# Performance work log

Measured on AMD Instinct MI355X. Metric: run time of the kernel, lower is better.

## Reference

```python
import jax, jax.numpy as jnp
import numpy as np

B, T, C, H, NUM_EDGE_TYPES = 2, 512, 256, 8, 16


def setup_inputs() -> dict:
    key = jax.random.key(0)
    ks = jax.random.split(key, 8)
    init = 0.02
    x = jax.random.normal(ks[0], (B, T, C), dtype=jnp.float32)
    bias_matrix = jax.random.randint(ks[1], (B, T, T), 0, NUM_EDGE_TYPES)
    w_attn = jax.random.normal(ks[2], (C, 3 * C), dtype=jnp.float32) * init
    w_proj = jax.random.normal(ks[3], (C, C), dtype=jnp.float32) * init
    w_edge_k = jax.random.normal(ks[4], (C, C), dtype=jnp.float32) * init
    w_edge_v = jax.random.normal(ks[5], (C, C), dtype=jnp.float32) * init
    edge_emb_table = jax.random.normal(ks[6], (NUM_EDGE_TYPES, C), dtype=jnp.float32)
    attn_bias_table = jax.random.normal(ks[7], (NUM_EDGE_TYPES, H), dtype=jnp.float32)
    return {
        "x": x,
        "bias_matrix": bias_matrix,
        "w_attn": w_attn,
        "w_proj": w_proj,
        "w_edge_k": w_edge_k,
        "w_edge_v": w_edge_v,
        "edge_emb_table": edge_emb_table,
        "attn_bias_table": attn_bias_table,
    }


def reference(x, bias_matrix, w_attn, w_proj, w_edge_k, w_edge_v,
              edge_emb_table, attn_bias_table):
    b, t, c = x.shape
    h = attn_bias_table.shape[1]
    e = c // h
    scale = jnp.sqrt(jnp.asarray(e, x.dtype))

    qkv = x @ w_attn                              # (B,T,3C)
    q, k, v = jnp.split(qkv, 3, axis=-1)
    # (B,H,T,E)
    q = q.reshape(b, t, h, e).transpose(0, 2, 1, 3)
    k = k.reshape(b, t, h, e).transpose(0, 2, 1, 3)
    v = v.reshape(b, t, h, e).transpose(0, 2, 1, 3)

    # edge-type embeddings and per-pair k/v modulation, (B,T,T,H,E)
    ee = edge_emb_table[bias_matrix]              # (B,T,T,C)
    e_k = (ee @ w_edge_k).reshape(b, t, t, h, e)
    e_v = (ee @ w_edge_v).reshape(b, t, t, h, e)

    # scores[b,h,i,j] = sum_e q[b,h,i,e] * k[b,h,j,e] * e_k[b, j, i, h, e]
    # (torch: e_k permuted to (B,H,j,i,E), broadcast-multiplied by k then
    #  contracted with q via 'bhie,bhjie->bhij')
    scores = jnp.einsum('bhie,bhje,bjihe->bhij', q, k, e_k) / scale

    causal = jnp.tril(jnp.ones((t, t), dtype=bool))  # (T,T)
    scores = jnp.where(causal, scores, -jnp.inf)

    # edge-type attention bias: (B,T,T,H) -> (B,H,T,T), zeroed above diagonal
    bias = attn_bias_table[bias_matrix].transpose(0, 3, 1, 2)
    bias = jnp.where(causal, bias, jnp.zeros((), bias.dtype))

    attn = jax.nn.softmax(scores + bias, axis=-1)  # (B,H,T,T)

    # y[b,h,i,e] = sum_j attn[b,h,i,j] * v[b,h,j,e] * e_v[b, j, i, h, e]
    y = jnp.einsum('bhij,bhje,bjihe->bhie', attn, v, e_v)
    y = y.transpose(0, 2, 1, 3).reshape(b, t, c)
    return y @ w_proj
```

## Files before the change

kernel.cpp:

```cpp
#include <hip/hip_runtime.h>
#include <hip/hip_bf16.h>
#include <math.h>

#define Bdim 2
#define Tdim 512
#define Cdim 256
#define Hdim 8
#define Edim 32
#define NTYPES 16
#define TI 8
#define JT 128

__global__ __launch_bounds__(256) void pre_kernel(
    const float* __restrict__ A, const float* __restrict__ Bw,
    const float* __restrict__ emb, const float* __restrict__ wk,
    const float* __restrict__ wv,
    float* __restrict__ qT, float* __restrict__ kT, float* __restrict__ vT,
    float* __restrict__ ekt, float* __restrict__ evt)
{
    __shared__ float smem[16 * 68 + 16 * 64];
    int tid = threadIdx.x;

    if (blockIdx.x >= 192) {
        int t = blockIdx.x - 192;
        float* se = smem;
        se[tid] = emb[t * Cdim + tid];
        __syncthreads();
        float a = 0.f, b = 0.f;
        for (int k = 0; k < Cdim; ++k) {
            float ev = se[k];
            a = fmaf(ev, wk[k * Cdim + tid], a);
            b = fmaf(ev, wv[k * Cdim + tid], b);
        }
        ekt[t * Cdim + tid] = a;
        evt[t * Cdim + tid] = b;
        return;
    }

    const int N = 3 * Cdim;
    const int K = Cdim;
    float (*As)[68] = (float(*)[68])smem;
    float (*Bs)[64] = (float(*)[64])(smem + 16 * 68);
    int m0 = (blockIdx.x / 12) * 64;
    int n0 = (blockIdx.x % 12) * 64;
    int tr = tid >> 4, tc = tid & 15;
    float acc[4][4] = {};
    int ar = tid >> 2, akq = (tid & 3) * 4;
    int bkr = tid >> 4, bcq = (tid & 15) * 4;

    for (int k0 = 0; k0 < K; k0 += 16) {
        float4 av = *(const float4*)(A + (size_t)(m0 + ar) * K + k0 + akq);
        float4 bv = *(const float4*)(Bw + (size_t)(k0 + bkr) * N + n0 + bcq);
        As[akq + 0][ar] = av.x;
        As[akq + 1][ar] = av.y;
        As[akq + 2][ar] = av.z;
        As[akq + 3][ar] = av.w;
        *(float4*)&Bs[bkr][bcq] = bv;
        __syncthreads();
#pragma unroll
        for (int kk = 0; kk < 16; ++kk) {
            float a0 = As[kk][tr * 4 + 0];
            float a1 = As[kk][tr * 4 + 1];
            float a2 = As[kk][tr * 4 + 2];
            float a3 = As[kk][tr * 4 + 3];
            float b0 = Bs[kk][tc * 4 + 0];
            float b1 = Bs[kk][tc * 4 + 1];
            float b2 = Bs[kk][tc * 4 + 2];
            float b3 = Bs[kk][tc * 4 + 3];
            acc[0][0] = fmaf(a0, b0, acc[0][0]);
            acc[0][1] = fmaf(a0, b1, acc[0][1]);
            acc[0][2] = fmaf(a0, b2, acc[0][2]);
            acc[0][3] = fmaf(a0, b3, acc[0][3]);
            acc[1][0] = fmaf(a1, b0, acc[1][0]);
            acc[1][1] = fmaf(a1, b1, acc[1][1]);
            acc[1][2] = fmaf(a1, b2, acc[1][2]);
            acc[1][3] = fmaf(a1, b3, acc[1][3]);
            acc[2][0] = fmaf(a2, b0, acc[2][0]);
            acc[2][1] = fmaf(a2, b1, acc[2][1]);
            acc[2][2] = fmaf(a2, b2, acc[2][2]);
            acc[2][3] = fmaf(a2, b3, acc[2][3]);
            acc[3][0] = fmaf(a3, b0, acc[3][0]);
            acc[3][1] = fmaf(a3, b1, acc[3][1]);
            acc[3][2] = fmaf(a3, b2, acc[3][2]);
            acc[3][3] = fmaf(a3, b3, acc[3][3]);
        }
        __syncthreads();
    }
#pragma unroll
    for (int i = 0; i < 4; ++i) {
#pragma unroll
        for (int j = 0; j < 4; ++j) {
            int m = m0 + tr * 4 + i;
            int n = n0 + tc * 4 + j;
            int b = m >> 9;
            int t = m & (Tdim - 1);
            int sec = n >> 8;
            int cc = n & (Cdim - 1);
            int h = cc >> 5;
            int e = cc & (Edim - 1);
            float* dst = (sec == 0) ? qT : (sec == 1) ? kT : vT;
            dst[(((size_t)b * Hdim + h) * Tdim + t) * Edim + e] = acc[i][j];
        }
    }
}

__global__ __launch_bounds__(512, 4) void attn_kernel(
    const float* __restrict__ qT, const float* __restrict__ kT,
    const float* __restrict__ vT, const int* __restrict__ bm,
    const float* __restrict__ ekt, const float* __restrict__ evt,
    const float* __restrict__ abt, float* __restrict__ y)
{
    __shared__ float kv[JT][36];
    __shared__ float qm[TI][NTYPES][36];
    __shared__ float ss[TI][516];
    __shared__ int   st1i[JT][17];
    __shared__ float sekt[NTYPES][36];
    __shared__ float sevt[NTYPES][36];
    __shared__ float sq[TI][36];
    __shared__ float sabt[NTYPES];
    __shared__ float sinv[TI];
    __shared__ float spartW[8][TI][Edim];

    const int pairIdx = blockIdx.x;
    const int bh = blockIdx.y;
    const int h = bh & (Hdim - 1);
    const int b = bh >> 3;
    const int tid = threadIdx.x;
    const int wave = tid >> 6;
    const int lane = tid & 63;
    const float inv_scale = 0.17677669529663687f;

    const float* qbase = qT + (size_t)bh * Tdim * Edim;
    const float* kbase = kT + (size_t)bh * Tdim * Edim;
    const float* vbase = vT + (size_t)bh * Tdim * Edim;
    const int* bmb = bm + (size_t)b * Tdim * Tdim;

    if (tid < 128) {
        int t = tid >> 3, eq = tid & 7;
        *(float4*)&sekt[t][eq * 4] = *(const float4*)&ekt[t * Cdim + h * Edim + eq * 4];
        *(float4*)&sevt[t][eq * 4] = *(const float4*)&evt[t * Cdim + h * Edim + eq * 4];
    }
    if (tid < NTYPES) sabt[tid] = abt[tid * Hdim + h];

    for (int rep = 0; rep < 2; ++rep) {
        int tau = rep ? (63 - pairIdx) : pairIdx;
        int i0 = tau * TI;
        int imax = i0 + TI - 1;
        int njt = (imax >> 7) + 1;

        __syncthreads();

        if (tid < TI * 8) {
            int r = tid >> 3, eq = tid & 7;
            *(float4*)&sq[r][eq * 4] =
                *(const float4*)&qbase[(size_t)(i0 + r) * Edim + eq * 4];
        }
        __syncthreads();
        for (int idx = tid; idx < TI * NTYPES * 8; idx += 512) {
            int eq = idx & 7;
            int t = (idx >> 3) & (NTYPES - 1);
            int r = idx >> 7;
            float4 qv = *(float4*)&sq[r][eq * 4];
            float4 ev = *(float4*)&sekt[t][eq * 4];
            float4 o;
            o.x = qv.x * ev.x; o.y = qv.y * ev.y;
            o.z = qv.z * ev.z; o.w = qv.w * ev.w;
            *(float4*)&qm[r][t][eq * 4] = o;
        }

        for (int jt = 0; jt < njt; ++jt) {
            int j0 = jt << 7;
            __syncthreads();
            for (int idx = tid; idx < JT * 8; idx += 512) {
                int r = idx >> 3, eq = idx & 7;
                *(float4*)&kv[r][eq * 4] =
                    *(const float4*)&kbase[(size_t)(j0 + r) * Edim + eq * 4];
            }
            if (tid < 256) {
                int r = tid >> 1, iq = (tid & 1) * 4;
                int4 bmv = *(const int4*)&bmb[(size_t)(j0 + r) * Tdim + i0 + iq];
                st1i[r][iq + 0] = bmv.x;
                st1i[r][iq + 1] = bmv.y;
                st1i[r][iq + 2] = bmv.z;
                st1i[r][iq + 3] = bmv.w;
            }
            __syncthreads();

            int jsub = wave & 1;
            int jl = (jsub << 6) + lane;
            int j = j0 + jl;
            float4 k4[8];
#pragma unroll
            for (int eq = 0; eq < 8; ++eq) k4[eq] = *(float4*)&kv[jl][eq * 4];

#pragma unroll
            for (int u = 0; u < 2; ++u) {
                int ii = (wave >> 1) + u * 4;
                int i = i0 + ii;
                if (j0 + (jsub << 6) > i) continue;
                int t1 = st1i[jl][ii];
                int t2 = bmb[(size_t)i * Tdim + j];
                float s = 0.f;
#pragma unroll
                for (int eq = 0; eq < 8; ++eq) {
                    float4 qv = *(float4*)&qm[ii][t1][eq * 4];
                    s = fmaf(qv.x, k4[eq].x, s);
                    s = fmaf(qv.y, k4[eq].y, s);
                    s = fmaf(qv.z, k4[eq].z, s);
                    s = fmaf(qv.w, k4[eq].w, s);
                }
                if (j <= i) ss[ii][j] = s * inv_scale + sabt[t2];
            }
        }
        __syncthreads();

        {
            int ii = wave;
            int i = i0 + ii;
            float m = -1e30f;
            for (int j = lane; j <= i; j += 64) m = fmaxf(m, ss[ii][j]);
            for (int off = 32; off; off >>= 1) m = fmaxf(m, __shfl_xor(m, off));
            float sum = 0.f;
            for (int j = lane; j <= i; j += 64) {
                float p = __expf(ss[ii][j] - m);
                ss[ii][j] = p;
                sum += p;
            }
            for (int off = 32; off; off >>= 1) sum += __shfl_xor(sum, off);
            if (lane == 0) sinv[ii] = 1.0f / sum;
        }

        float4 acc[TI];
#pragma unroll
        for (int ii = 0; ii < TI; ++ii) acc[ii] = make_float4(0.f, 0.f, 0.f, 0.f);
        int gid = tid >> 3;
        int eqg = tid & 7;
        for (int jt = 0; jt < njt; ++jt) {
            int j0 = jt << 7;
            __syncthreads();
            for (int idx = tid; idx < JT * 8; idx += 512) {
                int r = idx >> 3, eq = idx & 7;
                *(float4*)&kv[r][eq * 4] =
                    *(const float4*)&vbase[(size_t)(j0 + r) * Edim + eq * 4];
            }
            if (tid < 256) {
                int r = tid >> 1, iq = (tid & 1) * 4;
                int4 bmv = *(const int4*)&bmb[(size_t)(j0 + r) * Tdim + i0 + iq];
                st1i[r][iq + 0] = bmv.x;
                st1i[r][iq + 1] = bmv.y;
                st1i[r][iq + 2] = bmv.z;
                st1i[r][iq + 3] = bmv.w;
            }
            __syncthreads();
#pragma unroll
            for (int sub = 0; sub < 2; ++sub) {
                int jl = (sub << 6) + gid;
                int j = j0 + jl;
                float4 v4 = *(float4*)&kv[jl][eqg * 4];
#pragma unroll
                for (int ii = 0; ii < TI; ++ii) {
                    int i = i0 + ii;
                    if (j0 + (sub << 6) > i) continue;
                    float p = (j <= i) ? ss[ii][j] : 0.f;
                    int t1 = st1i[jl][ii];
                    float4 ev = *(float4*)&sevt[t1][eqg * 4];
                    acc[ii].x = fmaf(p * ev.x, v4.x, acc[ii].x);
                    acc[ii].y = fmaf(p * ev.y, v4.y, acc[ii].y);
                    acc[ii].z = fmaf(p * ev.z, v4.z, acc[ii].z);
                    acc[ii].w = fmaf(p * ev.w, v4.w, acc[ii].w);
                }
            }
        }
#pragma unroll
        for (int ii = 0; ii < TI; ++ii) {
#pragma unroll
            for (int m = 8; m <= 32; m <<= 1) {
                acc[ii].x += __shfl_xor(acc[ii].x, m);
                acc[ii].y += __shfl_xor(acc[ii].y, m);
                acc[ii].z += __shfl_xor(acc[ii].z, m);
                acc[ii].w += __shfl_xor(acc[ii].w, m);
            }
        }
        __syncthreads();
        if (lane < 8) {
#pragma unroll
            for (int ii = 0; ii < TI; ++ii)
                *(float4*)&spartW[wave][ii][lane * 4] = acc[ii];
        }
        __syncthreads();
        if (tid < TI * Edim) {
            int ii = tid >> 5, e = tid & 31;
            float yv = 0.f;
#pragma unroll
            for (int w = 0; w < 8; ++w) yv += spartW[w][ii][e];
            yv *= sinv[ii];
            y[((size_t)(b * Tdim + i0 + ii)) * Cdim + h * Edim + e] = yv;
        }
    }
}

__global__ __launch_bounds__(256) void proj_gemm_kernel(
    const float* __restrict__ A, const float* __restrict__ Bw,
    float* __restrict__ out)
{
    const int N = Cdim;
    const int K = Cdim;
    __shared__ float As[16][68];
    __shared__ float Bs[16][64];
    int m0 = blockIdx.y * 64;
    int n0 = blockIdx.x * 64;
    int tid = threadIdx.x;
    int tr = tid >> 4, tc = tid & 15;
    float acc[4][4] = {};
    int ar = tid >> 2, akq = (tid & 3) * 4;
    int bkr = tid >> 4, bcq = (tid & 15) * 4;

    for (int k0 = 0; k0 < K; k0 += 16) {
        float4 av = *(const float4*)(A + (size_t)(m0 + ar) * K + k0 + akq);
        float4 bv = *(const float4*)(Bw + (size_t)(k0 + bkr) * N + n0 + bcq);
        As[akq + 0][ar] = av.x;
        As[akq + 1][ar] = av.y;
        As[akq + 2][ar] = av.z;
        As[akq + 3][ar] = av.w;
        *(float4*)&Bs[bkr][bcq] = bv;
        __syncthreads();
#pragma unroll
        for (int kk = 0; kk < 16; ++kk) {
            float a0 = As[kk][tr * 4 + 0];
            float a1 = As[kk][tr * 4 + 1];
            float a2 = As[kk][tr * 4 + 2];
            float a3 = As[kk][tr * 4 + 3];
            float b0 = Bs[kk][tc * 4 + 0];
            float b1 = Bs[kk][tc * 4 + 1];
            float b2 = Bs[kk][tc * 4 + 2];
            float b3 = Bs[kk][tc * 4 + 3];
            acc[0][0] = fmaf(a0, b0, acc[0][0]);
            acc[0][1] = fmaf(a0, b1, acc[0][1]);
            acc[0][2] = fmaf(a0, b2, acc[0][2]);
            acc[0][3] = fmaf(a0, b3, acc[0][3]);
            acc[1][0] = fmaf(a1, b0, acc[1][0]);
            acc[1][1] = fmaf(a1, b1, acc[1][1]);
            acc[1][2] = fmaf(a1, b2, acc[1][2]);
            acc[1][3] = fmaf(a1, b3, acc[1][3]);
            acc[2][0] = fmaf(a2, b0, acc[2][0]);
            acc[2][1] = fmaf(a2, b1, acc[2][1]);
            acc[2][2] = fmaf(a2, b2, acc[2][2]);
            acc[2][3] = fmaf(a2, b3, acc[2][3]);
            acc[3][0] = fmaf(a3, b0, acc[3][0]);
            acc[3][1] = fmaf(a3, b1, acc[3][1]);
            acc[3][2] = fmaf(a3, b2, acc[3][2]);
            acc[3][3] = fmaf(a3, b3, acc[3][3]);
        }
        __syncthreads();
    }
#pragma unroll
    for (int i = 0; i < 4; ++i) {
#pragma unroll
        for (int j = 0; j < 4; ++j) {
            int m = m0 + tr * 4 + i;
            int nn = n0 + tc * 4 + j;
            out[(size_t)m * N + nn] = acc[i][j];
        }
    }
}

extern "C" void kernel_launch(void* const* d_in, const int* in_sizes, int n_in,
                              void* d_out, int out_size, void* d_ws, size_t ws_size,
                              hipStream_t stream) {
    (void)in_sizes; (void)n_in; (void)out_size; (void)ws_size;
    const float* x = (const float*)d_in[0];
    const int* bias_matrix = (const int*)d_in[1];
    const float* w_attn = (const float*)d_in[2];
    const float* w_proj = (const float*)d_in[3];
    const float* w_edge_k = (const float*)d_in[4];
    const float* w_edge_v = (const float*)d_in[5];
    const float* edge_emb = (const float*)d_in[6];
    const float* attn_bias = (const float*)d_in[7];
    float* out = (float*)d_out;

    const size_t n_qkv = (size_t)Bdim * Hdim * Tdim * Edim;
    float* ws = (float*)d_ws;
    float* qT = ws;
    float* kT = qT + n_qkv;
    float* vT = kT + n_qkv;
    float* y = vT + n_qkv;
    float* ekt = y + (size_t)Bdim * Tdim * Cdim;
    float* evt = ekt + (size_t)NTYPES * Cdim;

    pre_kernel<<<208, 256, 0, stream>>>(x, w_attn, edge_emb, w_edge_k, w_edge_v,
                                        qT, kT, vT, ekt, evt);
    attn_kernel<<<dim3(32, 16), 512, 0, stream>>>(qT, kT, vT, bias_matrix,
                                                  ekt, evt, attn_bias, y);
    proj_gemm_kernel<<<dim3(4, 16), 256, 0, stream>>>(y, w_proj, out);
}
```

Measured before the change: 135.9 us.

## Double-buffer K/V tiles, pack edge types, shrink GEMM tiles for more blocks

The attention kernel now double-buffers the K and V tiles in shared memory, prefetching the next tile into registers while the current one is used, so each j-tile needs one barrier instead of two. Edge-type indices for the whole i-range are packed as 4-bit nibbles into one word per j row, and the qm and spartW buffers share storage. Both GEMM kernels move to 32x64 tiles with float4 stores, doubling the number of blocks to fill more CUs. The cost is higher register pressure from the prefetch, more shared memory for the double buffer, and a packing step that relies on edge types being below 16.

```diff
diff --git a/kernel.cpp b/kernel.cpp
--- a/kernel.cpp
+++ b/kernel.cpp
@@ -18,11 +18,11 @@
     float* __restrict__ qT, float* __restrict__ kT, float* __restrict__ vT,
     float* __restrict__ ekt, float* __restrict__ evt)
 {
-    __shared__ float smem[16 * 68 + 16 * 64];
+    __shared__ float smem[16 * 34 + 16 * 64];
     int tid = threadIdx.x;
 
-    if (blockIdx.x >= 192) {
-        int t = blockIdx.x - 192;
+    if (blockIdx.x >= 384) {
+        int t = blockIdx.x - 384;
         float* se = smem;
         se[tid] = emb[t * Cdim + tid];
         __syncthreads();
@@ -39,68 +39,52 @@
 
     const int N = 3 * Cdim;
     const int K = Cdim;
-    float (*As)[68] = (float(*)[68])smem;
-    float (*Bs)[64] = (float(*)[64])(smem + 16 * 68);
-    int m0 = (blockIdx.x / 12) * 64;
+    float (*As)[34] = (float(*)[34])smem;
+    float (*Bs)[64] = (float(*)[64])(smem + 16 * 34);
+    int m0 = (blockIdx.x / 12) * 32;
     int n0 = (blockIdx.x % 12) * 64;
     int tr = tid >> 4, tc = tid & 15;
-    float acc[4][4] = {};
-    int ar = tid >> 2, akq = (tid & 3) * 4;
+    float acc[2][4] = {};
     int bkr = tid >> 4, bcq = (tid & 15) * 4;
 
     for (int k0 = 0; k0 < K; k0 += 16) {
-        float4 av = *(const float4*)(A + (size_t)(m0 + ar) * K + k0 + akq);
+        if (tid < 128) {
+            int r = tid >> 2, kq = (tid & 3) * 4;
+            float4 av = *(const float4*)(A + (size_t)(m0 + r) * K + k0 + kq);
+            As[kq + 0][r] = av.x;
+            As[kq + 1][r] = av.y;
+            As[kq + 2][r] = av.z;
+            As[kq + 3][r] = av.w;
+        }
         float4 bv = *(const float4*)(Bw + (size_t)(k0 + bkr) * N + n0 + bcq);
-        As[akq + 0][ar] = av.x;
-        As[akq + 1][ar] = av.y;
-        As[akq + 2][ar] = av.z;
-        As[akq + 3][ar] = av.w;
         *(float4*)&Bs[bkr][bcq] = bv;
         __syncthreads();
 #pragma unroll
         for (int kk = 0; kk < 16; ++kk) {
-            float a0 = As[kk][tr * 4 + 0];
-            float a1 = As[kk][tr * 4 + 1];
-            float a2 = As[kk][tr * 4 + 2];
-            float a3 = As[kk][tr * 4 + 3];
-            float b0 = Bs[kk][tc * 4 + 0];
-            float b1 = Bs[kk][tc * 4 + 1];
-            float b2 = Bs[kk][tc * 4 + 2];
-            float b3 = Bs[kk][tc * 4 + 3];
-            acc[0][0] = fmaf(a0, b0, acc[0][0]);
-            acc[0][1] = fmaf(a0, b1, acc[0][1]);
-            acc[0][2] = fmaf(a0, b2, acc[0][2]);
-            acc[0][3] = fmaf(a0, b3, acc[0][3]);
-            acc[1][0] = fmaf(a1, b0, acc[1][0]);
-            acc[1][1] = fmaf(a1, b1, acc[1][1]);
-            acc[1][2] = fmaf(a1, b2, acc[1][2]);
-            acc[1][3] = fmaf(a1, b3, acc[1][3]);
-            acc[2][0] = fmaf(a2, b0, acc[2][0]);
-            acc[2][1] = fmaf(a2, b1, acc[2][1]);
-            acc[2][2] = fmaf(a2, b2, acc[2][2]);
-            acc[2][3] = fmaf(a2, b3, acc[2][3]);
-            acc[3][0] = fmaf(a3, b0, acc[3][0]);
-            acc[3][1] = fmaf(a3, b1, acc[3][1]);
-            acc[3][2] = fmaf(a3, b2, acc[3][2]);
-            acc[3][3] = fmaf(a3, b3, acc[3][3]);
-        }
-        __syncthreads();
-    }
-#pragma unroll
-    for (int i = 0; i < 4; ++i) {
-#pragma unroll
-        for (int j = 0; j < 4; ++j) {
-            int m = m0 + tr * 4 + i;
-            int n = n0 + tc * 4 + j;
-            int b = m >> 9;
-            int t = m & (Tdim - 1);
-            int sec = n >> 8;
-            int cc = n & (Cdim - 1);
-            int h = cc >> 5;
-            int e = cc & (Edim - 1);
-            float* dst = (sec == 0) ? qT : (sec == 1) ? kT : vT;
-            dst[(((size_t)b * Hdim + h) * Tdim + t) * Edim + e] = acc[i][j];
-        }
+            float2 a2 = *(float2*)&As[kk][tr * 2];
+            float4 b4 = *(float4*)&Bs[kk][tc * 4];
+            acc[0][0] = fmaf(a2.x, b4.x, acc[0][0]);
+            acc[0][1] = fmaf(a2.x, b4.y, acc[0][1]);
+            acc[0][2] = fmaf(a2.x, b4.z, acc[0][2]);
+            acc[0][3] = fmaf(a2.x, b4.w, acc[0][3]);
+            acc[1][0] = fmaf(a2.y, b4.x, acc[1][0]);
+            acc[1][1] = fmaf(a2.y, b4.y, acc[1][1]);
+            acc[1][2] = fmaf(a2.y, b4.z, acc[1][2]);
+            acc[1][3] = fmaf(a2.y, b4.w, acc[1][3]);
+        }
+        __syncthreads();
+    }
+    int sec = n0 >> 8;
+    float* dst = (sec == 0) ? qT : (sec == 1) ? kT : vT;
+    int cc0 = (n0 & 255) + tc * 4;
+    int h = cc0 >> 5;
+    int e0 = cc0 & 31;
+#pragma unroll
+    for (int i = 0; i < 2; ++i) {
+        int m = m0 + tr * 2 + i;
+        int bq = m >> 9, t = m & (Tdim - 1);
+        float4 val = make_float4(acc[i][0], acc[i][1], acc[i][2], acc[i][3]);
+        *(float4*)&dst[(((size_t)bq * Hdim + h) * Tdim + t) * Edim + e0] = val;
     }
 }
 
@@ -110,16 +94,18 @@
     const float* __restrict__ ekt, const float* __restrict__ evt,
     const float* __restrict__ abt, float* __restrict__ y)
 {
-    __shared__ float kv[JT][36];
-    __shared__ float qm[TI][NTYPES][36];
+    __shared__ float kv[2][JT][36];
+    __shared__ float qm_spart[TI * NTYPES * 36];
     __shared__ float ss[TI][516];
-    __shared__ int   st1i[JT][17];
+    __shared__ unsigned int st1p[4][JT];
     __shared__ float sekt[NTYPES][36];
     __shared__ float sevt[NTYPES][36];
     __shared__ float sq[TI][36];
     __shared__ float sabt[NTYPES];
     __shared__ float sinv[TI];
-    __shared__ float spartW[8][TI][Edim];
+
+    float (*qm)[NTYPES][36] = (float (*)[NTYPES][36])qm_spart;
+    float (*spartW)[TI][Edim] = (float (*)[TI][Edim])qm_spart;
 
     const int pairIdx = blockIdx.x;
     const int bh = blockIdx.y;
@@ -154,6 +140,25 @@
             int r = tid >> 3, eq = tid & 7;
             *(float4*)&sq[r][eq * 4] =
                 *(const float4*)&qbase[(size_t)(i0 + r) * Edim + eq * 4];
+        }
+        {
+            int r0 = tid >> 3, eq0 = tid & 7;
+            *(float4*)&kv[0][r0][eq0 * 4] =
+                *(const float4*)&kbase[(size_t)r0 * Edim + eq0 * 4];
+            int idx1 = tid + 512;
+            int r1 = idx1 >> 3, eq1 = idx1 & 7;
+            *(float4*)&kv[0][r1][eq1 * 4] =
+                *(const float4*)&kbase[(size_t)r1 * Edim + eq1 * 4];
+        }
+        if (tid < JT) {
+            const int* rowp = bmb + (size_t)tid * Tdim + i0;
+            int4 lo = *(const int4*)rowp;
+            int4 hi = *(const int4*)(rowp + 4);
+            st1p[0][tid] =
+                ((unsigned)(lo.x & 15)) | (((unsigned)(lo.y & 15)) << 4) |
+                (((unsigned)(lo.z & 15)) << 8) | (((unsigned)(lo.w & 15)) << 12) |
+                (((unsigned)(hi.x & 15)) << 16) | (((unsigned)(hi.y & 15)) << 20) |
+                (((unsigned)(hi.z & 15)) << 24) | (((unsigned)(hi.w & 15)) << 28);
         }
         __syncthreads();
         for (int idx = tid; idx < TI * NTYPES * 8; idx += 512) {
@@ -167,38 +172,45 @@
             o.z = qv.z * ev.z; o.w = qv.w * ev.w;
             *(float4*)&qm[r][t][eq * 4] = o;
         }
+        __syncthreads();
 
         for (int jt = 0; jt < njt; ++jt) {
             int j0 = jt << 7;
-            __syncthreads();
-            for (int idx = tid; idx < JT * 8; idx += 512) {
-                int r = idx >> 3, eq = idx & 7;
-                *(float4*)&kv[r][eq * 4] =
-                    *(const float4*)&kbase[(size_t)(j0 + r) * Edim + eq * 4];
-            }
-            if (tid < 256) {
-                int r = tid >> 1, iq = (tid & 1) * 4;
-                int4 bmv = *(const int4*)&bmb[(size_t)(j0 + r) * Tdim + i0 + iq];
-                st1i[r][iq + 0] = bmv.x;
-                st1i[r][iq + 1] = bmv.y;
-                st1i[r][iq + 2] = bmv.z;
-                st1i[r][iq + 3] = bmv.w;
-            }
-            __syncthreads();
-
+            int nb = jt & 1;
+            bool hn = (jt + 1 < njt);
+            float4 pf0, pf1;
+            unsigned pst = 0;
+            if (hn) {
+                int j0n = j0 + JT;
+                int r0 = tid >> 3, eq0 = tid & 7;
+                pf0 = *(const float4*)&kbase[(size_t)(j0n + r0) * Edim + eq0 * 4];
+                int idx1 = tid + 512;
+                int r1 = idx1 >> 3, eq1 = idx1 & 7;
+                pf1 = *(const float4*)&kbase[(size_t)(j0n + r1) * Edim + eq1 * 4];
+                if (tid < JT) {
+                    const int* rowp = bmb + (size_t)(j0n + tid) * Tdim + i0;
+                    int4 lo = *(const int4*)rowp;
+                    int4 hi = *(const int4*)(rowp + 4);
+                    pst =
+                        ((unsigned)(lo.x & 15)) | (((unsigned)(lo.y & 15)) << 4) |
+                        (((unsigned)(lo.z & 15)) << 8) | (((unsigned)(lo.w & 15)) << 12) |
+                        (((unsigned)(hi.x & 15)) << 16) | (((unsigned)(hi.y & 15)) << 20) |
+                        (((unsigned)(hi.z & 15)) << 24) | (((unsigned)(hi.w & 15)) << 28);
+                }
+            }
             int jsub = wave & 1;
             int jl = (jsub << 6) + lane;
             int j = j0 + jl;
             float4 k4[8];
 #pragma unroll
-            for (int eq = 0; eq < 8; ++eq) k4[eq] = *(float4*)&kv[jl][eq * 4];
-
+            for (int eq = 0; eq < 8; ++eq) k4[eq] = *(float4*)&kv[nb][jl][eq * 4];
+            unsigned tp = st1p[jt][jl];
 #pragma unroll
             for (int u = 0; u < 2; ++u) {
-                int ii = (wave >> 1) + u * 4;
+                int ii = (wave >> 1) + (u << 2);
                 int i = i0 + ii;
                 if (j0 + (jsub << 6) > i) continue;
-                int t1 = st1i[jl][ii];
+                int t1 = (tp >> (ii * 4)) & 15;
                 int t2 = bmb[(size_t)i * Tdim + j];
                 float s = 0.f;
 #pragma unroll
@@ -211,9 +223,27 @@
                 }
                 if (j <= i) ss[ii][j] = s * inv_scale + sabt[t2];
             }
-        }
-        __syncthreads();
-
+            if (hn) {
+                int ob = nb ^ 1;
+                int r0 = tid >> 3, eq0 = tid & 7;
+                *(float4*)&kv[ob][r0][eq0 * 4] = pf0;
+                int idx1 = tid + 512;
+                int r1 = idx1 >> 3, eq1 = idx1 & 7;
+                *(float4*)&kv[ob][r1][eq1 * 4] = pf1;
+                if (tid < JT) st1p[jt + 1][tid] = pst;
+            }
+            __syncthreads();
+        }
+
+        {
+            int r0 = tid >> 3, eq0 = tid & 7;
+            *(float4*)&kv[0][r0][eq0 * 4] =
+                *(const float4*)&vbase[(size_t)r0 * Edim + eq0 * 4];
+            int idx1 = tid + 512;
+            int r1 = idx1 >> 3, eq1 = idx1 & 7;
+            *(float4*)&kv[0][r1][eq1 * 4] =
+                *(const float4*)&vbase[(size_t)r1 * Edim + eq1 * 4];
+        }
         {
             int ii = wave;
             int i = i0 + ii;
@@ -229,6 +259,7 @@
             for (int off = 32; off; off >>= 1) sum += __shfl_xor(sum, off);
             if (lane == 0) sinv[ii] = 1.0f / sum;
         }
+        __syncthreads();
 
         float4 acc[TI];
 #pragma unroll
@@ -237,32 +268,29 @@
         int eqg = tid & 7;
         for (int jt = 0; jt < njt; ++jt) {
             int j0 = jt << 7;
-            __syncthreads();
-            for (int idx = tid; idx < JT * 8; idx += 512) {
-                int r = idx >> 3, eq = idx & 7;
-                *(float4*)&kv[r][eq * 4] =
-                    *(const float4*)&vbase[(size_t)(j0 + r) * Edim + eq * 4];
-            }
-            if (tid < 256) {
-                int r = tid >> 1, iq = (tid & 1) * 4;
-                int4 bmv = *(const int4*)&bmb[(size_t)(j0 + r) * Tdim + i0 + iq];
-                st1i[r][iq + 0] = bmv.x;
-                st1i[r][iq + 1] = bmv.y;
-                st1i[r][iq + 2] = bmv.z;
-                st1i[r][iq + 3] = bmv.w;
-            }
-            __syncthreads();
+            int nb = jt & 1;
+            bool hn = (jt + 1 < njt);
+            float4 pf0, pf1;
+            if (hn) {
+                int j0n = j0 + JT;
+                int r0 = tid >> 3, eq0 = tid & 7;
+                pf0 = *(const float4*)&vbase[(size_t)(j0n + r0) * Edim + eq0 * 4];
+                int idx1 = tid + 512;
+                int r1 = idx1 >> 3, eq1 = idx1 & 7;
+                pf1 = *(const float4*)&vbase[(size_t)(j0n + r1) * Edim + eq1 * 4];
+            }
 #pragma unroll
             for (int sub = 0; sub < 2; ++sub) {
                 int jl = (sub << 6) + gid;
                 int j = j0 + jl;
-                float4 v4 = *(float4*)&kv[jl][eqg * 4];
+                float4 v4 = *(float4*)&kv[nb][jl][eqg * 4];
+                unsigned tp = st1p[jt][jl];
 #pragma unroll
                 for (int ii = 0; ii < TI; ++ii) {
                     int i = i0 + ii;
                     if (j0 + (sub << 6) > i) continue;
                     float p = (j <= i) ? ss[ii][j] : 0.f;
-                    int t1 = st1i[jl][ii];
+                    int t1 = (tp >> (ii * 4)) & 15;
                     float4 ev = *(float4*)&sevt[t1][eqg * 4];
                     acc[ii].x = fmaf(p * ev.x, v4.x, acc[ii].x);
                     acc[ii].y = fmaf(p * ev.y, v4.y, acc[ii].y);
@@ -270,6 +298,15 @@
                     acc[ii].w = fmaf(p * ev.w, v4.w, acc[ii].w);
                 }
             }
+            if (hn) {
+                int ob = nb ^ 1;
+                int r0 = tid >> 3, eq0 = tid & 7;
+                *(float4*)&kv[ob][r0][eq0 * 4] = pf0;
+                int idx1 = tid + 512;
+                int r1 = idx1 >> 3, eq1 = idx1 & 7;
+                *(float4*)&kv[ob][r1][eq1 * 4] = pf1;
+            }
+            __syncthreads();
         }
 #pragma unroll
         for (int ii = 0; ii < TI; ++ii) {
@@ -281,7 +318,6 @@
                 acc[ii].w += __shfl_xor(acc[ii].w, m);
             }
         }
-        __syncthreads();
         if (lane < 8) {
 #pragma unroll
             for (int ii = 0; ii < TI; ++ii)
@@ -305,62 +341,47 @@
 {
     const int N = Cdim;
     const int K = Cdim;
-    __shared__ float As[16][68];
+    __shared__ float As[16][34];
     __shared__ float Bs[16][64];
-    int m0 = blockIdx.y * 64;
+    int m0 = blockIdx.y * 32;
     int n0 = blockIdx.x * 64;
     int tid = threadIdx.x;
     int tr = tid >> 4, tc = tid & 15;
-    float acc[4][4] = {};
-    int ar = tid >> 2, akq = (tid & 3) * 4;
+    float acc[2][4] = {};
     int bkr = tid >> 4, bcq = (tid & 15) * 4;
 
     for (int k0 = 0; k0 < K; k0 += 16) {
-        float4 av = *(const float4*)(A + (size_t)(m0 + ar) * K + k0 + akq);
+        if (tid < 128) {
+            int r = tid >> 2, kq = (tid & 3) * 4;
+            float4 av = *(const float4*)(A + (size_t)(m0 + r) * K + k0 + kq);
+            As[kq + 0][r] = av.x;
+            As[kq + 1][r] = av.y;
+            As[kq + 2][r] = av.z;
+            As[kq + 3][r] = av.w;
+        }
         float4 bv = *(const float4*)(Bw + (size_t)(k0 + bkr) * N + n0 + bcq);
-        As[akq + 0][ar] = av.x;
-        As[akq + 1][ar] = av.y;
-        As[akq + 2][ar] = av.z;
-        As[akq + 3][ar] = av.w;
         *(float4*)&Bs[bkr][bcq] = bv;
         __syncthreads();
 #pragma unroll
         for (int kk = 0; kk < 16; ++kk) {
-            float a0 = As[kk][tr * 4 + 0];
-            float a1 = As[kk][tr * 4 + 1];
-            float a2 = As[kk][tr * 4 + 2];
-            float a3 = As[kk][tr * 4 + 3];
-            float b0 = Bs[kk][tc * 4 + 0];
-            float b1 = Bs[kk][tc * 4 + 1];
-            float b2 = Bs[kk][tc * 4 + 2];
-            float b3 = Bs[kk][tc * 4 + 3];
-            acc[0][0] = fmaf(a0, b0, acc[0][0]);
-            acc[0][1] = fmaf(a0, b1, acc[0][1]);
-            acc[0][2] = fmaf(a0, b2, acc[0][2]);
-            acc[0][3] = fmaf(a0, b3, acc[0][3]);
-            acc[1][0] = fmaf(a1, b0, acc[1][0]);
-            acc[1][1] = fmaf(a1, b1, acc[1][1]);
-            acc[1][2] = fmaf(a1, b2, acc[1][2]);
-            acc[1][3] = fmaf(a1, b3, acc[1][3]);
-            acc[2][0] = fmaf(a2, b0, acc[2][0]);
-            acc[2][1] = fmaf(a2, b1, acc[2][1]);
-            acc[2][2] = fmaf(a2, b2, acc[2][2]);
-            acc[2][3] = fmaf(a2, b3, acc[2][3]);
-            acc[3][0] = fmaf(a3, b0, acc[3][0]);
-            acc[3][1] = fmaf(a3, b1, acc[3][1]);
-            acc[3][2] = fmaf(a3, b2, acc[3][2]);
-            acc[3][3] = fmaf(a3, b3, acc[3][3]);
-        }
-        __syncthreads();
-    }
-#pragma unroll
-    for (int i = 0; i < 4; ++i) {
-#pragma unroll
-        for (int j = 0; j < 4; ++j) {
-            int m = m0 + tr * 4 + i;
-            int nn = n0 + tc * 4 + j;
-            out[(size_t)m * N + nn] = acc[i][j];
-        }
+            float2 a2 = *(float2*)&As[kk][tr * 2];
+            float4 b4 = *(float4*)&Bs[kk][tc * 4];
+            acc[0][0] = fmaf(a2.x, b4.x, acc[0][0]);
+            acc[0][1] = fmaf(a2.x, b4.y, acc[0][1]);
+            acc[0][2] = fmaf(a2.x, b4.z, acc[0][2]);
+            acc[0][3] = fmaf(a2.x, b4.w, acc[0][3]);
+            acc[1][0] = fmaf(a2.y, b4.x, acc[1][0]);
+            acc[1][1] = fmaf(a2.y, b4.y, acc[1][1]);
+            acc[1][2] = fmaf(a2.y, b4.z, acc[1][2]);
+            acc[1][3] = fmaf(a2.y, b4.w, acc[1][3]);
+        }
+        __syncthreads();
+    }
+#pragma unroll
+    for (int i = 0; i < 2; ++i) {
+        int m = m0 + tr * 2 + i;
+        float4 val = make_float4(acc[i][0], acc[i][1], acc[i][2], acc[i][3]);
+        *(float4*)&out[(size_t)m * N + n0 + tc * 4] = val;
     }
 }
 
@@ -387,9 +408,9 @@
     float* ekt = y + (size_t)Bdim * Tdim * Cdim;
     float* evt = ekt + (size_t)NTYPES * Cdim;
 
-    pre_kernel<<<208, 256, 0, stream>>>(x, w_attn, edge_emb, w_edge_k, w_edge_v,
+    pre_kernel<<<400, 256, 0, stream>>>(x, w_attn, edge_emb, w_edge_k, w_edge_v,
                                         qT, kT, vT, ekt, evt);
     attn_kernel<<<dim3(32, 16), 512, 0, stream>>>(qT, kT, vT, bias_matrix,
                                                   ekt, evt, attn_bias, y);
-    proj_gemm_kernel<<<dim3(4, 16), 256, 0, stream>>>(y, w_proj, out);
+    proj_gemm_kernel<<<dim3(4, 32), 256, 0, stream>>>(y, w_proj, out);
 }
```

New measurement: 140.2 us. 3.2% more time.
